# Performance work log

Measured on AMD Instinct MI355X. Metric: run time of the kernel, lower is better.

## Reference

```python
import jax, jax.numpy as jnp
import numpy as np

D_MODEL = 64  # angle_dist_dim
IN_CH = 256
EPS = 1e-6


def sinusoidal_embedding(e, d_model):
    # e: (N, K) -> (N, K, d_model), interleaved [sin0, cos0, sin1, cos1, ...]
    div_term = jnp.exp(jnp.arange(0, d_model, 2, dtype=jnp.float32) * (-np.log(10000.0) / d_model))
    om = e[..., None] * div_term  # (N, K, d_model//2)
    emb = jnp.stack([jnp.sin(om), jnp.cos(om)], axis=-1)  # (N, K, d/2, 2)
    return emb.reshape(e.shape + (d_model,))


def setup_inputs() -> dict:
    key = jax.random.key(0)
    ks = jax.random.split(key, 5)
    N, K, C = 40000, 16, IN_CH
    triplet_dim = 2 * C + D_MODEL  # 576
    x = jax.random.normal(ks[0], (N, C), dtype=jnp.float32)
    pos = jax.random.normal(ks[1], (N, 3), dtype=jnp.float32) * 10.0
    anchor_indices = jnp.arange(N, dtype=jnp.int32)
    corner_indices = jax.random.randint(ks[2], (N, K, 2), 0, N, dtype=jnp.int32)
    corner_masks = jnp.ones((N, K), dtype=bool)
    Wqkv_w = jax.random.normal(ks[3], (3 * C, triplet_dim), dtype=jnp.float32) / np.sqrt(triplet_dim)
    Wqkv_b = jax.random.normal(ks[4], (3 * C,), dtype=jnp.float32) * 0.01
    return {"x": x, "pos": pos, "anchor_indices": anchor_indices,
            "corner_indices": corner_indices, "corner_masks": corner_masks,
            "Wqkv_w": Wqkv_w, "Wqkv_b": Wqkv_b}


def reference(x, pos, anchor_indices, corner_indices, corner_masks, Wqkv_w, Wqkv_b):
    N, C = x.shape
    padded_x = jnp.concatenate([x, jnp.zeros((1, C), x.dtype)], axis=0)
    padded_pos = jnp.concatenate([pos, jnp.zeros((1, 3), pos.dtype)], axis=0)

    anchor_p = padded_pos[anchor_indices]            # (Na, 3)
    v0 = padded_pos[corner_indices[:, :, 0]] - anchor_p[:, None]  # (Na, K, 3)
    v1 = padded_pos[corner_indices[:, :, 1]] - anchor_p[:, None]
    v0 = jax.lax.stop_gradient(v0).at[:, :, 2].set(0.0)  # zero z (detached geometry)
    v1 = jax.lax.stop_gradient(v1).at[:, :, 2].set(0.0)

    cos_values = jnp.sum(v0 * v1, axis=-1) / (
        jnp.linalg.norm(v0, axis=-1) * jnp.linalg.norm(v1, axis=-1) + EPS)
    # z-component of cross product (x,y only since z was zeroed)
    sin_z = v0[..., 0] * v1[..., 1] - v0[..., 1] * v1[..., 0]
    reorder = sin_z < 0  # (Na, K)

    ci = jnp.where(reorder[..., None], corner_indices[:, :, ::-1], corner_indices)

    nv0 = jax.lax.stop_gradient(padded_pos[ci[:, :, 0]] - anchor_p[:, None]).at[:, :, 2].set(0.0)
    nv1 = jax.lax.stop_gradient(padded_pos[ci[:, :, 1]] - anchor_p[:, None]).at[:, :, 2].set(0.0)
    new_sin_z = nv0[..., 0] * nv1[..., 1] - nv0[..., 1] * nv1[..., 0]
    # corner_masks is all-True so boolean selection == full flatten (static shape)
    triplet_false_masks = ((new_sin_z < -1e-6) & corner_masks).reshape(-1)

    angle_features = jax.lax.stop_gradient(sinusoidal_embedding(cos_values, D_MODEL))
    triplet_feats = jnp.concatenate(
        [padded_x[ci[:, :, 0]], padded_x[ci[:, :, 1]], angle_features], axis=-1)  # (Na, K, 576)

    qkv = triplet_feats @ Wqkv_w.T + Wqkv_b            # (Na, K, 3C)
    qkv = qkv.reshape(qkv.shape[0], qkv.shape[1], 3, C)
    q, k, v = qkv[:, :, 0], qkv[:, :, 1], qkv[:, :, 2]

    scores = jnp.einsum('nqc,nkc->nqk', q, k) / np.sqrt(C)
    attn = jax.nn.softmax(scores, axis=-1)
    attn_feats = jnp.einsum('nqk,nkc->nqc', attn, v)   # (Na, K, C)

    mask_f = corner_masks.astype(attn_feats.dtype)
    denom = jnp.sum(mask_f, axis=1, keepdims=True)     # (Na, 1)
    mean_feats = jnp.sum(attn_feats * mask_f[..., None], axis=1) / denom  # (Na, C)

    x_messages = jnp.zeros_like(x).at[anchor_indices].set(mean_feats)
    out = jnp.concatenate([x, x_messages], axis=1)     # (N, 2C), triplet_mlp_method='concat'
    return out, triplet_false_masks
```

## Files before the change

kernel.cpp:

```cpp
#include <hip/hip_runtime.h>

typedef unsigned short u16;
typedef __attribute__((ext_vector_type(8))) short short8v;
typedef __attribute__((ext_vector_type(4))) float float4v;

__device__ __forceinline__ float bf2f(u16 u) {
  union { unsigned int i; float f; } v; v.i = ((unsigned int)u) << 16; return v.f;
}
__device__ __forceinline__ u16 f2bf(float f) {
  union { unsigned int i; float f; } v; v.f = f;
  unsigned int r = v.i + 0x7fffu + ((v.i >> 16) & 1u);
  return (u16)(r >> 16);
}
__device__ __forceinline__ float4v mfma_bf16(short8v a, short8v b, float4v c) {
  return __builtin_amdgcn_mfma_f32_16x16x32_bf16(a, b, c, 0, 0, 0);
}

__global__ __launch_bounds__(256) void prep_kernel(const float* __restrict__ W,
                                                   u16* __restrict__ Bt,
                                                   u16* __restrict__ W2t) {
  int j = blockIdx.x;
  int c = threadIdx.x;
  const float* wr = W + (size_t)j * 576;
  Bt[(size_t)j * 256 + c]         = f2bf(wr[c]);
  Bt[(size_t)(768 + j) * 256 + c] = f2bf(wr[256 + c]);
  if (c < 64) W2t[(size_t)j * 64 + c] = f2bf(wr[512 + c]);
}

__global__ __launch_bounds__(256) void gemm_kernel(const float* __restrict__ A,
                                                   const u16* __restrict__ Bt,
                                                   u16* __restrict__ Y, int M) {
  __shared__ __align__(16) u16 As[128][72];
  __shared__ __align__(16) u16 Bs[128][72];
  int tid = threadIdx.x;
  int row0 = blockIdx.x * 128, col0 = blockIdx.y * 128;
  int w = tid >> 6, l = tid & 63;
  int wr = w >> 1, wc = w & 1;
  int lr = l & 15, lq = l >> 4;

  float4v acc[4][4];
#pragma unroll
  for (int mi = 0; mi < 4; mi++)
#pragma unroll
    for (int ni = 0; ni < 4; ni++) acc[mi][ni] = (float4v)0.f;

  for (int k0 = 0; k0 < 256; k0 += 64) {
#pragma unroll
    for (int i = 0; i < 4; i++) {
      int chunk = tid + i * 256;
      int r = chunk >> 3;
      int kc = (chunk & 7) * 8;
      int gr = row0 + r;
      short8v av = (short8v)0;
      if (gr < M) {
        float4 f0 = *(const float4*)(A + (size_t)gr * 256 + k0 + kc);
        float4 f1 = *(const float4*)(A + (size_t)gr * 256 + k0 + kc + 4);
        av[0] = (short)f2bf(f0.x); av[1] = (short)f2bf(f0.y);
        av[2] = (short)f2bf(f0.z); av[3] = (short)f2bf(f0.w);
        av[4] = (short)f2bf(f1.x); av[5] = (short)f2bf(f1.y);
        av[6] = (short)f2bf(f1.z); av[7] = (short)f2bf(f1.w);
      }
      *(short8v*)&As[r][kc] = av;
      short8v bv = *(const short8v*)(Bt + (size_t)(col0 + r) * 256 + k0 + kc);
      *(short8v*)&Bs[r][kc] = bv;
    }
    __syncthreads();
#pragma unroll
    for (int s = 0; s < 2; s++) {
      int kb = s * 32 + lq * 8;
      short8v af[4], bf[4];
#pragma unroll
      for (int mi = 0; mi < 4; mi++)
        af[mi] = *(const short8v*)&As[wr * 64 + mi * 16 + lr][kb];
#pragma unroll
      for (int ni = 0; ni < 4; ni++)
        bf[ni] = *(const short8v*)&Bs[wc * 64 + ni * 16 + lr][kb];
#pragma unroll
      for (int mi = 0; mi < 4; mi++)
#pragma unroll
        for (int ni = 0; ni < 4; ni++)
          acc[mi][ni] = mfma_bf16(af[mi], bf[ni], acc[mi][ni]);
    }
    __syncthreads();
  }
#pragma unroll
  for (int mi = 0; mi < 4; mi++)
#pragma unroll
    for (int ni = 0; ni < 4; ni++) {
      int rbase = row0 + wr * 64 + mi * 16 + lq * 4;
      int c = col0 + wc * 64 + ni * 16 + lr;
#pragma unroll
      for (int j = 0; j < 4; j++) {
        int r = rbase + j;
        if (r < M) Y[(size_t)r * 1536 + c] = f2bf(acc[mi][ni][j]);
      }
    }
}

__global__ __launch_bounds__(64) void triplet_kernel(
    const float* __restrict__ x, const float* __restrict__ pos,
    const int* __restrict__ anchor, const int* __restrict__ corner,
    const float* __restrict__ bias, const u16* __restrict__ Y,
    const u16* __restrict__ W2t, float* __restrict__ out, int N) {
  __shared__ float s_cos[16];
  __shared__ int s_i0[16], s_i1[16];
  __shared__ __align__(16) u16 s_qkv[16][776];

  int n = blockIdx.x;
  if (n >= N) return;
  int l = threadIdx.x;
  int lr = l & 15, lq = l >> 4, kg = lq * 8;
  int a = anchor[n];

  if (l < 16) {
    int t = l;
    int2 ci = ((const int2*)corner)[n * 16 + t];
    float ax = pos[(size_t)a * 3], ay = pos[(size_t)a * 3 + 1];
    float v0x = pos[(size_t)ci.x * 3]     - ax;
    float v0y = pos[(size_t)ci.x * 3 + 1] - ay;
    float v1x = pos[(size_t)ci.y * 3]     - ax;
    float v1y = pos[(size_t)ci.y * 3 + 1] - ay;
    float dot = v0x * v1x + v0y * v1y;
    float n0 = sqrtf(v0x * v0x + v0y * v0y);
    float n1 = sqrtf(v1x * v1x + v1y * v1y);
    s_cos[t] = dot / (n0 * n1 + 1e-6f);
    float sinz = v0x * v1y - v0y * v1x;
    bool sw = sinz < 0.f;
    s_i0[t] = sw ? ci.y : ci.x;
    s_i1[t] = sw ? ci.x : ci.y;
    out[(size_t)N * 512 + (size_t)n * 16 + t] = 0.0f;
  }
  {
    float4 v = ((const float4*)(x + (size_t)n * 256))[l];
    ((float4*)(out + (size_t)n * 512))[l] = v;
  }
  __syncthreads();

  float cosv = s_cos[lr];
  short8v a0, a1;
#pragma unroll
  for (int j = 0; j < 8; j++) {
    int k = kg + j;
    float dv0 = __expf(-0.28782313662425572f * (float)(k >> 1));
    float om0 = cosv * dv0;
    float f0 = (k & 1) ? __cosf(om0) : __sinf(om0);
    a0[j] = (short)f2bf(f0);
    int k2 = 32 + kg + j;
    float dv1 = __expf(-0.28782313662425572f * (float)(k2 >> 1));
    float om1 = cosv * dv1;
    float f1 = (k2 & 1) ? __cosf(om1) : __sinf(om1);
    a1[j] = (short)f2bf(f1);
  }
  int i0r[4], i1r[4];
#pragma unroll
  for (int j = 0; j < 4; j++) {
    int t = lq * 4 + j;
    i0r[j] = s_i0[t];
    i1r[j] = s_i1[t];
  }

  for (int nt = 0; nt < 48; nt++) {
    int col = nt * 16 + lr;
    short8v b0 = *(const short8v*)(W2t + (size_t)col * 64 + kg);
    short8v b1 = *(const short8v*)(W2t + (size_t)col * 64 + 32 + kg);
    float4v acc = (float4v)0.f;
    acc = mfma_bf16(a0, b0, acc);
    acc = mfma_bf16(a1, b1, acc);
    float bs = bias[col];
#pragma unroll
    for (int j = 0; j < 4; j++) {
      float v = acc[j] + bs + bf2f(Y[(size_t)i0r[j] * 1536 + col]) +
                bf2f(Y[(size_t)i1r[j] * 1536 + 768 + col]);
      s_qkv[lq * 4 + j][col] = f2bf(v);
    }
  }
  __syncthreads();

  float4v sa = (float4v)0.f;
#pragma unroll
  for (int cs = 0; cs < 8; cs++) {
    short8v qf = *(const short8v*)&s_qkv[lr][cs * 32 + kg];
    short8v kf = *(const short8v*)&s_qkv[lr][256 + cs * 32 + kg];
    sa = mfma_bf16(qf, kf, sa);
  }
  float wsum = 0.f;
#pragma unroll
  for (int j = 0; j < 4; j++) {
    float s = sa[j] * 0.0625f;
    float m = s;
    m = fmaxf(m, __shfl_xor(m, 1));
    m = fmaxf(m, __shfl_xor(m, 2));
    m = fmaxf(m, __shfl_xor(m, 4));
    m = fmaxf(m, __shfl_xor(m, 8));
    float e = __expf(s - m);
    float sm = e;
    sm += __shfl_xor(sm, 1);
    sm += __shfl_xor(sm, 2);
    sm += __shfl_xor(sm, 4);
    sm += __shfl_xor(sm, 8);
    wsum += e / sm;
  }
  wsum += __shfl_xor(wsum, 16);
  wsum += __shfl_xor(wsum, 32);
  wsum *= 0.0625f;

  float o0 = 0.f, o1 = 0.f, o2 = 0.f, o3 = 0.f;
#pragma unroll
  for (int kk = 0; kk < 16; kk++) {
    float wk = __shfl(wsum, kk);
    ushort4 v4 = *(const ushort4*)&s_qkv[kk][512 + l * 4];
    o0 += wk * bf2f(v4.x);
    o1 += wk * bf2f(v4.y);
    o2 += wk * bf2f(v4.z);
    o3 += wk * bf2f(v4.w);
  }
  float4 ov; ov.x = o0; ov.y = o1; ov.z = o2; ov.w = o3;
  ((float4*)(out + (size_t)a * 512 + 256))[l] = ov;
}

extern "C" void kernel_launch(void* const* d_in, const int* in_sizes, int n_in,
                              void* d_out, int out_size, void* d_ws, size_t ws_size,
                              hipStream_t stream) {
  const float* x    = (const float*)d_in[0];
  const float* pos  = (const float*)d_in[1];
  const int* anchor = (const int*)d_in[2];
  const int* corner = (const int*)d_in[3];
  const float* W    = (const float*)d_in[5];
  const float* bias = (const float*)d_in[6];
  float* out = (float*)d_out;
  int N = in_sizes[2];

  char* wsb = (char*)d_ws;
  u16* Bt  = (u16*)wsb;
  u16* W2t = (u16*)(wsb + 786432);
  u16* Y   = (u16*)(wsb + 786432 + 98304);

  prep_kernel<<<768, 256, 0, stream>>>(W, Bt, W2t);
  gemm_kernel<<<dim3((N + 127) / 128, 12), 256, 0, stream>>>(x, Bt, Y, N);
  triplet_kernel<<<N, 64, 0, stream>>>(x, pos, anchor, corner, bias, Y, W2t, out, N);
}
```

Measured before the change: 869.4 us.

## Stream QKV per channel chunk through small LDS tile instead of full qkv buffer

The triplet kernel no longer builds the full 16x768 bf16 qkv tile in shared memory. It computes the angle-feature projection in 32-channel chunks, staging only a 16x64 tile. Q/K are assembled in registers from that tile, the bias and the gathered Y rows, then fed straight into the score MFMA. V is handled the same way in a second chunked pass, reduced with shuffles, so LDS use drops from about 25KB to about 2KB per block and more blocks can be resident. It also makes the gathered Y reads vectorized 16-byte row loads, has every lane compute the geometry instead of one staging pass through shared memory, and adds a launch-bounds occupancy hint. The cost is many more block barriers, plus shuffle reductions and mostly idle lanes on the output stores.

```diff
diff --git a/kernel.cpp b/kernel.cpp
--- a/kernel.cpp
+++ b/kernel.cpp
@@ -97,14 +97,12 @@
     }
 }
 
-__global__ __launch_bounds__(64) void triplet_kernel(
+__global__ __launch_bounds__(64, 4) void triplet_kernel(
     const float* __restrict__ x, const float* __restrict__ pos,
     const int* __restrict__ anchor, const int* __restrict__ corner,
     const float* __restrict__ bias, const u16* __restrict__ Y,
     const u16* __restrict__ W2t, float* __restrict__ out, int N) {
-  __shared__ float s_cos[16];
-  __shared__ int s_i0[16], s_i1[16];
-  __shared__ __align__(16) u16 s_qkv[16][776];
+  __shared__ __align__(16) u16 s_t[16][72];
 
   int n = blockIdx.x;
   if (n >= N) return;
@@ -112,81 +110,83 @@
   int lr = l & 15, lq = l >> 4, kg = lq * 8;
   int a = anchor[n];
 
-  if (l < 16) {
-    int t = l;
-    int2 ci = ((const int2*)corner)[n * 16 + t];
-    float ax = pos[(size_t)a * 3], ay = pos[(size_t)a * 3 + 1];
-    float v0x = pos[(size_t)ci.x * 3]     - ax;
-    float v0y = pos[(size_t)ci.x * 3 + 1] - ay;
-    float v1x = pos[(size_t)ci.y * 3]     - ax;
-    float v1y = pos[(size_t)ci.y * 3 + 1] - ay;
-    float dot = v0x * v1x + v0y * v1y;
-    float n0 = sqrtf(v0x * v0x + v0y * v0y);
-    float n1 = sqrtf(v1x * v1x + v1y * v1y);
-    s_cos[t] = dot / (n0 * n1 + 1e-6f);
-    float sinz = v0x * v1y - v0y * v1x;
-    bool sw = sinz < 0.f;
-    s_i0[t] = sw ? ci.y : ci.x;
-    s_i1[t] = sw ? ci.x : ci.y;
-    out[(size_t)N * 512 + (size_t)n * 16 + t] = 0.0f;
-  }
+  int2 ci = ((const int2*)corner)[n * 16 + lr];
+  float ax = pos[(size_t)a * 3], ay = pos[(size_t)a * 3 + 1];
+  float v0x = pos[(size_t)ci.x * 3]     - ax;
+  float v0y = pos[(size_t)ci.x * 3 + 1] - ay;
+  float v1x = pos[(size_t)ci.y * 3]     - ax;
+  float v1y = pos[(size_t)ci.y * 3 + 1] - ay;
+  float dotv = v0x * v1x + v0y * v1y;
+  float n0 = sqrtf(v0x * v0x + v0y * v0y);
+  float n1 = sqrtf(v1x * v1x + v1y * v1y);
+  float cosv = dotv / (n0 * n1 + 1e-6f);
+  bool sw = (v0x * v1y - v0y * v1x) < 0.f;
+  int i0 = sw ? ci.y : ci.x;
+  int i1 = sw ? ci.x : ci.y;
+
+  if (l < 16) out[(size_t)N * 512 + (size_t)n * 16 + l] = 0.0f;
   {
     float4 v = ((const float4*)(x + (size_t)n * 256))[l];
     ((float4*)(out + (size_t)n * 512))[l] = v;
   }
-  __syncthreads();
-
-  float cosv = s_cos[lr];
+
   short8v a0, a1;
 #pragma unroll
   for (int j = 0; j < 8; j++) {
     int k = kg + j;
-    float dv0 = __expf(-0.28782313662425572f * (float)(k >> 1));
-    float om0 = cosv * dv0;
-    float f0 = (k & 1) ? __cosf(om0) : __sinf(om0);
-    a0[j] = (short)f2bf(f0);
+    float om0 = cosv * __expf(-0.28782313662425572f * (float)(k >> 1));
+    a0[j] = (short)f2bf((k & 1) ? __cosf(om0) : __sinf(om0));
     int k2 = 32 + kg + j;
-    float dv1 = __expf(-0.28782313662425572f * (float)(k2 >> 1));
-    float om1 = cosv * dv1;
-    float f1 = (k2 & 1) ? __cosf(om1) : __sinf(om1);
-    a1[j] = (short)f2bf(f1);
-  }
-  int i0r[4], i1r[4];
+    float om1 = cosv * __expf(-0.28782313662425572f * (float)(k2 >> 1));
+    a1[j] = (short)f2bf((k2 & 1) ? __cosf(om1) : __sinf(om1));
+  }
+
+  const u16* y0 = Y + (size_t)i0 * 1536;
+  const u16* y1 = Y + (size_t)i1 * 1536 + 768;
+
+  float4v sacc = (float4v)0.f;
+  for (int cs = 0; cs < 8; cs++) {
+    __syncthreads();
+#pragma unroll
+    for (int gi = 0; gi < 4; gi++) {
+      int g = (gi < 2) ? (cs * 2 + gi) : (16 + cs * 2 + (gi - 2));
+      const u16* wrow = W2t + (size_t)(g * 16 + lr) * 64;
+      short8v wa = *(const short8v*)(wrow + kg);
+      short8v wb = *(const short8v*)(wrow + 32 + kg);
+      float4v d = mfma_bf16(wb, a1, (float4v)0.f);
+      d = mfma_bf16(wa, a0, d);
+      uint2 pv;
+      pv.x = (unsigned)f2bf(d[0]) | ((unsigned)f2bf(d[1]) << 16);
+      pv.y = (unsigned)f2bf(d[2]) | ((unsigned)f2bf(d[3]) << 16);
+      *(uint2*)&s_t[lr][gi * 16 + lq * 4] = pv;
+    }
+    __syncthreads();
+    int cq = cs * 32 + kg;
+    int ck = 256 + cs * 32 + kg;
+    short8v tq = *(const short8v*)&s_t[lr][kg];
+    short8v tk = *(const short8v*)&s_t[lr][32 + kg];
+    short8v gq0 = *(const short8v*)(y0 + cq);
+    short8v gq1 = *(const short8v*)(y1 + cq);
+    short8v gk0 = *(const short8v*)(y0 + ck);
+    short8v gk1 = *(const short8v*)(y1 + ck);
+    union { float4 v[2]; float f[8]; } bq, bk;
+    bq.v[0] = *(const float4*)(bias + cq); bq.v[1] = *(const float4*)(bias + cq + 4);
+    bk.v[0] = *(const float4*)(bias + ck); bk.v[1] = *(const float4*)(bias + ck + 4);
+    short8v qf, kf;
+#pragma unroll
+    for (int j = 0; j < 8; j++) {
+      float qv = bf2f((u16)tq[j]) + bq.f[j] + bf2f((u16)gq0[j]) + bf2f((u16)gq1[j]);
+      qf[j] = (short)f2bf(qv);
+      float kv = bf2f((u16)tk[j]) + bk.f[j] + bf2f((u16)gk0[j]) + bf2f((u16)gk1[j]);
+      kf[j] = (short)f2bf(kv);
+    }
+    sacc = mfma_bf16(qf, kf, sacc);
+  }
+
+  float wsum = 0.f;
 #pragma unroll
   for (int j = 0; j < 4; j++) {
-    int t = lq * 4 + j;
-    i0r[j] = s_i0[t];
-    i1r[j] = s_i1[t];
-  }
-
-  for (int nt = 0; nt < 48; nt++) {
-    int col = nt * 16 + lr;
-    short8v b0 = *(const short8v*)(W2t + (size_t)col * 64 + kg);
-    short8v b1 = *(const short8v*)(W2t + (size_t)col * 64 + 32 + kg);
-    float4v acc = (float4v)0.f;
-    acc = mfma_bf16(a0, b0, acc);
-    acc = mfma_bf16(a1, b1, acc);
-    float bs = bias[col];
-#pragma unroll
-    for (int j = 0; j < 4; j++) {
-      float v = acc[j] + bs + bf2f(Y[(size_t)i0r[j] * 1536 + col]) +
-                bf2f(Y[(size_t)i1r[j] * 1536 + 768 + col]);
-      s_qkv[lq * 4 + j][col] = f2bf(v);
-    }
-  }
-  __syncthreads();
-
-  float4v sa = (float4v)0.f;
-#pragma unroll
-  for (int cs = 0; cs < 8; cs++) {
-    short8v qf = *(const short8v*)&s_qkv[lr][cs * 32 + kg];
-    short8v kf = *(const short8v*)&s_qkv[lr][256 + cs * 32 + kg];
-    sa = mfma_bf16(qf, kf, sa);
-  }
-  float wsum = 0.f;
-#pragma unroll
-  for (int j = 0; j < 4; j++) {
-    float s = sa[j] * 0.0625f;
+    float s = sacc[j] * 0.0625f;
     float m = s;
     m = fmaxf(m, __shfl_xor(m, 1));
     m = fmaxf(m, __shfl_xor(m, 2));
@@ -204,18 +204,48 @@
   wsum += __shfl_xor(wsum, 32);
   wsum *= 0.0625f;
 
-  float o0 = 0.f, o1 = 0.f, o2 = 0.f, o3 = 0.f;
-#pragma unroll
-  for (int kk = 0; kk < 16; kk++) {
-    float wk = __shfl(wsum, kk);
-    ushort4 v4 = *(const ushort4*)&s_qkv[kk][512 + l * 4];
-    o0 += wk * bf2f(v4.x);
-    o1 += wk * bf2f(v4.y);
-    o2 += wk * bf2f(v4.z);
-    o3 += wk * bf2f(v4.w);
-  }
-  float4 ov; ov.x = o0; ov.y = o1; ov.z = o2; ov.w = o3;
-  ((float4*)(out + (size_t)a * 512 + 256))[l] = ov;
+  float* op = out + (size_t)a * 512 + 256;
+  for (int cs = 0; cs < 8; cs++) {
+    __syncthreads();
+#pragma unroll
+    for (int gi = 0; gi < 2; gi++) {
+      int g = 32 + cs * 2 + gi;
+      const u16* wrow = W2t + (size_t)(g * 16 + lr) * 64;
+      short8v wa = *(const short8v*)(wrow + kg);
+      short8v wb = *(const short8v*)(wrow + 32 + kg);
+      float4v d = mfma_bf16(wb, a1, (float4v)0.f);
+      d = mfma_bf16(wa, a0, d);
+      uint2 pv;
+      pv.x = (unsigned)f2bf(d[0]) | ((unsigned)f2bf(d[1]) << 16);
+      pv.y = (unsigned)f2bf(d[2]) | ((unsigned)f2bf(d[3]) << 16);
+      *(uint2*)&s_t[lr][gi * 16 + lq * 4] = pv;
+    }
+    __syncthreads();
+    int cv = 512 + cs * 32 + kg;
+    short8v tv = *(const short8v*)&s_t[lr][kg];
+    short8v gv0 = *(const short8v*)(y0 + cv);
+    short8v gv1 = *(const short8v*)(y1 + cv);
+    union { float4 v[2]; float f[8]; } bv;
+    bv.v[0] = *(const float4*)(bias + cv); bv.v[1] = *(const float4*)(bias + cv + 4);
+    float o[8];
+#pragma unroll
+    for (int j = 0; j < 8; j++) {
+      float vv = bf2f((u16)tv[j]) + bv.f[j] + bf2f((u16)gv0[j]) + bf2f((u16)gv1[j]);
+      float p = wsum * vv;
+      p += __shfl_xor(p, 1);
+      p += __shfl_xor(p, 2);
+      p += __shfl_xor(p, 4);
+      p += __shfl_xor(p, 8);
+      o[j] = p;
+    }
+    if (lr == 0) {
+      float4 o0, o1;
+      o0.x = o[0]; o0.y = o[1]; o0.z = o[2]; o0.w = o[3];
+      o1.x = o[4]; o1.y = o[5]; o1.z = o[6]; o1.w = o[7];
+      *(float4*)(op + cs * 32 + kg) = o0;
+      *(float4*)(op + cs * 32 + kg + 4) = o1;
+    }
+  }
 }
 
 extern "C" void kernel_launch(void* const* d_in, const int* in_sizes, int n_in,
```

Result: slower. 904.6 us (+4.0%).
